# Optimization experiments

Measured on AMD Instinct MI355X. Metric: run time of the kernel, lower is better.

## Reference

```python
import jax, jax.numpy as jnp
import numpy as np

D_IN, D, K, N_CLASSES = 384, 512, 6, 2
SCALE = D ** (-0.5)

def _linear_params(key, fan_in, fan_out):
    kw, kb = jax.random.split(key)
    w = jax.random.normal(kw, (fan_in, fan_out), jnp.float32) * 0.02
    b = jax.random.normal(kb, (fan_out,), jnp.float32) * 0.01
    return w, b

def setup_inputs() -> dict:
    key = jax.random.key(0)
    ks = jax.random.split(key, 10)
    x = jax.random.normal(ks[0], (16384, D_IN), jnp.float32)
    fc1_w, fc1_b = _linear_params(ks[1], D_IN, D)
    wh_w, wh_b = _linear_params(ks[2], D, D)
    wt_w, wt_b = _linear_params(ks[3], D, D)
    lin1_w, lin1_b = _linear_params(ks[4], D, D)
    lin2_w, lin2_b = _linear_params(ks[5], D, D)
    att1_w, att1_b = _linear_params(ks[6], D, D // 2)
    att2_w, att2_b = _linear_params(ks[7], D // 2, 1)
    ln_g = jnp.ones((D,), jnp.float32)
    ln_b = jnp.zeros((D,), jnp.float32)
    fc_w, fc_b = _linear_params(ks[8], D, N_CLASSES)
    return dict(x=x, fc1_w=fc1_w, fc1_b=fc1_b, wh_w=wh_w, wh_b=wh_b,
                wt_w=wt_w, wt_b=wt_b, lin1_w=lin1_w, lin1_b=lin1_b,
                lin2_w=lin2_w, lin2_b=lin2_b, att1_w=att1_w, att1_b=att1_b,
                att2_w=att2_w, att2_b=att2_b, ln_g=ln_g, ln_b=ln_b,
                fc_w=fc_w, fc_b=fc_b)

def _forward(x, fc1_w, fc1_b, wh_w, wh_b, wt_w, wt_b, lin1_w, lin1_b,
             lin2_w, lin2_b, att1_w, att1_b, att2_w, att2_b, ln_g, ln_b,
             fc_w, fc_b):
    lrelu = jax.nn.leaky_relu  # slope 0.01, matches nn.LeakyReLU default
    h = lrelu(x @ fc1_w + fc1_b)                    # [N, D]
    h = (h + h.mean(axis=0, keepdims=True)) * 0.5
    e_h = h @ wh_w + wh_b                           # [N, D]
    e_t = h @ wt_w + wt_b                           # [N, D]
    attn_logit = (e_h * SCALE) @ e_t.T              # [N, N]
    topk_w, topk_i = jax.lax.top_k(attn_logit, K)   # [N, K]
    Nb = e_t[topk_i]                                # gather neighbors [N, K, D]
    p = jax.nn.softmax(topk_w, axis=-1)             # [N, K]
    eh_r = p[..., None] * Nb + (1.0 - p)[..., None] * e_h[:, None, :]
    gate = jnp.tanh(e_h[:, None, :] + eh_r)         # [N, K, D]
    # faithful to torch.einsum('ijkl,ijkm->ijk', Nb, gate): product of sums
    ka_w = Nb.sum(axis=-1) * gate.sum(axis=-1)      # [N, K]
    ka_p = jax.nn.softmax(ka_w, axis=-1)
    e_Nh = jnp.einsum('nk,nkd->nd', ka_p, Nb)       # [N, D]
    sum_emb = lrelu((e_h + e_Nh) @ lin1_w + lin1_b)
    bi_emb = lrelu((e_h * e_Nh) @ lin2_w + lin2_b)
    emb = sum_emb + bi_emb                          # [N, D] (dropout=eval, identity)
    # GlobalAttention readout
    a = lrelu(emb @ att1_w + att1_b) @ att2_w + att2_b  # [N, 1]
    g = jax.nn.softmax(a, axis=0)
    pooled = (g * emb).sum(axis=0, keepdims=True)   # [1, D]
    mu = pooled.mean(axis=-1, keepdims=True)
    var = pooled.var(axis=-1, keepdims=True)
    normed = (pooled - mu) * jax.lax.rsqrt(var + 1e-5) * ln_g + ln_b
    logits = normed @ fc_w + fc_b                   # [1, n_classes]
    return logits

def reference(x, fc1_w, fc1_b, wh_w, wh_b, wt_w, wt_b, lin1_w, lin1_b,
              lin2_w, lin2_b, att1_w, att1_b, att2_w, att2_b, ln_g, ln_b,
              fc_w, fc_b):
    logits = _forward(x, fc1_w, fc1_b, wh_w, wh_b, wt_w, wt_b, lin1_w, lin1_b,
                      lin2_w, lin2_b, att1_w, att1_b, att2_w, att2_b,
                      ln_g, ln_b, fc_w, fc_b)
    y_prob = jax.nn.softmax(logits, axis=-1)
    return logits, y_prob
```

## Files before the change

### kernel.cpp

```cpp
#include <hip/hip_runtime.h>
#include <math.h>

#define NROWS 16384
#define DIN   384
#define DIM   512
#define KSEL  6
#define NSPLIT 4
#define COLS_PER_SPLIT (NROWS / NSPLIT)
#define ATT_SCALE 0.044194173824159216f

typedef unsigned short u16;
typedef __attribute__((ext_vector_type(8))) short bf16x8;
typedef __attribute__((ext_vector_type(16))) float f32x16;

static __device__ __forceinline__ float lrelu_f(float v) {
  return v > 0.f ? v : 0.01f * v;
}

static __device__ __forceinline__ u16 f2bf(float f) {
  unsigned u = __float_as_uint(f);
  unsigned r = (u + 0x7FFFu + ((u >> 16) & 1u)) >> 16;
  return (u16)r;
}

static __device__ __forceinline__ void sbar() {
  asm volatile("" ::: "memory");
  __builtin_amdgcn_s_barrier();
  asm volatile("" ::: "memory");
}

__global__ __launch_bounds__(256)
void convx(const float* __restrict__ X, u16* __restrict__ Xb) {
  int i = blockIdx.x * 256 + threadIdx.x;
  const float4* p = (const float4*)X + (size_t)i * 2;
  float4 a = p[0], b = p[1];
  uint4 o;
  o.x = f2bf(a.x) | ((unsigned)f2bf(a.y) << 16);
  o.y = f2bf(a.z) | ((unsigned)f2bf(a.w) << 16);
  o.z = f2bf(b.x) | ((unsigned)f2bf(b.y) << 16);
  o.w = f2bf(b.z) | ((unsigned)f2bf(b.w) << 16);
  ((uint4*)Xb)[i] = o;
}

__global__ __launch_bounds__(256)
void wconv(const float* __restrict__ W, u16* __restrict__ Wt, int K, int N) {
  int t = blockIdx.x * 256 + threadIdx.x;
  if (t >= K * N) return;
  int k = t / N, n = t - k * N;
  Wt[(size_t)n * K + k] = f2bf(W[t]);
}

__global__ __launch_bounds__(256)
void colsum_partial(const float* __restrict__ H, float* __restrict__ part) {
  int col = blockIdx.x * 64 + (threadIdx.x & 63);
  int sub = threadIdx.x >> 6;
  int rEnd = blockIdx.y * 512 + 512;
  float s = 0.f;
  for (int r = blockIdx.y * 512 + sub; r < rEnd; r += 4)
    s += H[(size_t)r * DIM + col];
  __shared__ float sh[4][64];
  sh[sub][threadIdx.x & 63] = s;
  __syncthreads();
  if (threadIdx.x < 64) {
    float tot = sh[0][threadIdx.x] + sh[1][threadIdx.x] +
                sh[2][threadIdx.x] + sh[3][threadIdx.x];
    part[(size_t)blockIdx.y * DIM + col] = tot;
  }
}

__global__ void finalize_mean(const float* __restrict__ part,
                              float* __restrict__ mean) {
  int c = threadIdx.x;
  float s = 0.f;
  for (int j = 0; j < 32; j++) s += part[j * DIM + c];
  mean[c] = s * (1.0f / NROWS);
}

__global__ __launch_bounds__(256)
void h_fix_bf(const float* __restrict__ H0, const float* __restrict__ mean,
              u16* __restrict__ Hb) {
  int idx = blockIdx.x * 256 + threadIdx.x;
  int c = (idx * 8) & (DIM - 1);
  const float4* p = (const float4*)H0 + (size_t)idx * 2;
  float4 a = p[0], b = p[1];
  float4 m0 = *(const float4*)(mean + c);
  float4 m1 = *(const float4*)(mean + c + 4);
  a.x = (a.x + m0.x) * 0.5f; a.y = (a.y + m0.y) * 0.5f;
  a.z = (a.z + m0.z) * 0.5f; a.w = (a.w + m0.w) * 0.5f;
  b.x = (b.x + m1.x) * 0.5f; b.y = (b.y + m1.y) * 0.5f;
  b.z = (b.z + m1.z) * 0.5f; b.w = (b.w + m1.w) * 0.5f;
  uint4 o;
  o.x = f2bf(a.x) | ((unsigned)f2bf(a.y) << 16);
  o.y = f2bf(a.z) | ((unsigned)f2bf(a.w) << 16);
  o.z = f2bf(b.x) | ((unsigned)f2bf(b.y) << 16);
  o.w = f2bf(b.z) | ((unsigned)f2bf(b.w) << 16);
  ((uint4*)Hb)[idx] = o;
}

template<int ACT, int ACCUM, int STOREBF>
__global__ __launch_bounds__(256, 2)
void gemm_bf16(const u16* __restrict__ A, const u16* __restrict__ Wt,
               const float* __restrict__ bias, float* __restrict__ C,
               u16* __restrict__ Cb, float bscale, int K, int N) {
  __shared__ char lds[65536];
  const int tid = threadIdx.x;
  const int w = tid >> 6, l = tid & 63;
  const int l31 = l & 31, lh = l >> 5, lh16 = lh << 4;
  const int qg = w & 1, ng = w >> 1;
  const int swz = (l31 & 7) << 4;
  const int rowBase = blockIdx.y * 128;
  const int colBase = blockIdx.x * 128;
  const int nsteps = K >> 6;

  f32x16 z;
  #pragma unroll
  for (int i = 0; i < 16; i++) z[i] = 0.f;
  f32x16 acc00 = z, acc01 = z, acc10 = z, acc11 = z;

#define GSTAGE(buf_, kc_) do { \
    const int r_ = tid >> 3, j_ = tid & 7; \
    const int js_ = ((j_ ^ (r_ & 7)) << 3); \
    const u16* as_ = A + (size_t)rowBase * K + (kc_); \
    const u16* ws_ = Wt + (size_t)colBase * K + (kc_); \
    char* ab_ = lds + (buf_) * 16384; \
    char* wb_ = lds + 32768 + (buf_) * 16384; \
    _Pragma("unroll") \
    for (int p_ = 0; p_ < 4; ++p_) { \
      __builtin_amdgcn_global_load_lds( \
        (const __attribute__((address_space(1))) void*)(as_ + (size_t)(r_ + 32 * p_) * K + js_), \
        (__attribute__((address_space(3))) void*)(ab_ + w * 1024 + p_ * 4096), 16, 0, 0); \
      __builtin_amdgcn_global_load_lds( \
        (const __attribute__((address_space(1))) void*)(ws_ + (size_t)(r_ + 32 * p_) * K + js_), \
        (__attribute__((address_space(3))) void*)(wb_ + w * 1024 + p_ * 4096), 16, 0, 0); \
    } \
  } while (0)

  GSTAGE(0, 0);
  asm volatile("s_waitcnt vmcnt(0)" ::: "memory");
  sbar();
  #pragma unroll 1
  for (int s = 0; s < nsteps; ++s) {
    const int cur = s & 1;
    if (s + 1 < nsteps) GSTAGE(cur ^ 1, (s + 1) * 64);
    __builtin_amdgcn_sched_barrier(0);
    const char* ab = lds + cur * 16384;
    const char* wb = lds + 32768 + cur * 16384;
    __builtin_amdgcn_s_setprio(1);
    #pragma unroll
    for (int s4 = 0; s4 < 4; ++s4) {
      const int off = (s4 * 32 + lh16) ^ swz;
      bf16x8 am0 = *(const bf16x8*)(ab + (qg * 64 + l31) * 128 + off);
      bf16x8 am1 = *(const bf16x8*)(ab + (qg * 64 + 32 + l31) * 128 + off);
      bf16x8 wn0 = *(const bf16x8*)(wb + (ng * 64 + l31) * 128 + off);
      bf16x8 wn1 = *(const bf16x8*)(wb + (ng * 64 + 32 + l31) * 128 + off);
      acc00 = __builtin_amdgcn_mfma_f32_32x32x16_bf16(wn0, am0, acc00, 0, 0, 0);
      acc01 = __builtin_amdgcn_mfma_f32_32x32x16_bf16(wn1, am0, acc01, 0, 0, 0);
      acc10 = __builtin_amdgcn_mfma_f32_32x32x16_bf16(wn0, am1, acc10, 0, 0, 0);
      acc11 = __builtin_amdgcn_mfma_f32_32x32x16_bf16(wn1, am1, acc11, 0, 0, 0);
    }
    __builtin_amdgcn_s_setprio(0);
    asm volatile("s_waitcnt vmcnt(0)" ::: "memory");
    sbar();
  }
#undef GSTAGE

  float* Ls = (float*)lds;
  {
    const int m0 = qg * 64 + l31;
    const int k0 = (m0 & 7) << 2;
    #pragma unroll
    for (int r = 0; r < 16; ++r) {
      const int nd = ng * 64 + (r & 3) + 8 * (r >> 2) + 4 * lh;
      Ls[m0 * 128 + (nd ^ k0)] = acc00[r];
      Ls[m0 * 128 + ((nd + 32) ^ k0)] = acc01[r];
      Ls[(m0 + 32) * 128 + (nd ^ k0)] = acc10[r];
      Ls[(m0 + 32) * 128 + ((nd + 32) ^ k0)] = acc11[r];
    }
  }
  sbar();
  #pragma unroll
  for (int p = 0; p < 16; ++p) {
    int idx = tid + 256 * p;
    int m = idx >> 5, c4 = (idx & 31) << 2;
    float4 v = *(const float4*)&Ls[m * 128 + (c4 ^ ((m & 7) << 2))];
    int col = colBase + c4;
    float4 bv = *(const float4*)&bias[col];
    v.x += bv.x; v.y += bv.y; v.z += bv.z; v.w += bv.w;
    if (ACT) {
      v.x = lrelu_f(v.x); v.y = lrelu_f(v.y);
      v.z = lrelu_f(v.z); v.w = lrelu_f(v.w);
    }
    size_t o = (size_t)(rowBase + m) * N + col;
    if (ACCUM) {
      float4 c0 = *(const float4*)&C[o];
      v.x += c0.x; v.y += c0.y; v.z += c0.z; v.w += c0.w;
    }
    *(float4*)&C[o] = v;
    if (STOREBF) {
      ushort4 q;
      q.x = f2bf(v.x * bscale); q.y = f2bf(v.y * bscale);
      q.z = f2bf(v.z * bscale); q.w = f2bf(v.w * bscale);
      *(ushort4*)&Cb[o] = q;
    }
  }
}

#define T6(tv, tix, vv, cc) do { float v_ = (vv); \
  if (v_ > tv[5]) { tv[5] = v_; tix[5] = (cc); \
    if (tv[5] > tv[4]) { float t=tv[4];tv[4]=tv[5];tv[5]=t; int q=tix[4];tix[4]=tix[5];tix[5]=q; } \
    if (tv[4] > tv[3]) { float t=tv[3];tv[3]=tv[4];tv[4]=t; int q=tix[3];tix[3]=tix[4];tix[4]=q; } \
    if (tv[3] > tv[2]) { float t=tv[2];tv[2]=tv[3];tv[3]=t; int q=tix[2];tix[2]=tix[3];tix[3]=q; } \
    if (tv[2] > tv[1]) { float t=tv[1];tv[1]=tv[2];tv[2]=t; int q=tix[1];tix[1]=tix[2];tix[2]=q; } \
    if (tv[1] > tv[0]) { float t=tv[0];tv[0]=tv[1];tv[1]=t; int q=tix[0];tix[0]=tix[1];tix[1]=q; } \
  } } while (0)

__global__ __launch_bounds__(256, 2)
void attn_topk_mfma(const u16* __restrict__ EHb, const u16* __restrict__ ETb,
                    float* __restrict__ TWp, int* __restrict__ TIp) {
  __shared__ char lds[65536];
  const int tid = threadIdx.x;
  const int w = tid >> 6, l = tid & 63;
  const int l31 = l & 31, lh = l >> 5;

  const int bid = blockIdx.x;
  const int xcd = bid & 7;
  const int split = xcd & 3;
  const int rowBase = ((xcd >> 2) * 64 + (bid >> 3)) * 128;
  const int qrow = rowBase + w * 32 + l31;

  bf16x8 areg[32];
  {
    const u16* ap = EHb + (size_t)qrow * DIM + lh * 8;
    #pragma unroll
    for (int ks = 0; ks < 32; ++ks)
      areg[ks] = *(const bf16x8*)(ap + ks * 16);
  }

  char* ldsw = lds + w * 16384;

  f32x16 z;
  #pragma unroll
  for (int i = 0; i < 16; i++) z[i] = 0.f;
  f32x16 acc0 = z, acc1 = z;

  float tv[KSEL]; int tix[KSEL];
  #pragma unroll
  for (int k = 0; k < KSEL; k++) { tv[k] = -INFINITY; tix[k] = 0x7fffffff; }

#define STAGE(buf_, ct_, kc_) do { \
    char* db_ = ldsw + (buf_) * 8192; \
    const u16* bs_ = ETb + (size_t)(split * COLS_PER_SPLIT + (ct_) * 64) * DIM + (kc_) * 64; \
    _Pragma("unroll") \
    for (int p_ = 0; p_ < 8; ++p_) { \
      const int rn_ = p_ * 8 + (l >> 3); \
      const int js_ = ((l & 7) ^ (rn_ & 7)) * 8; \
      __builtin_amdgcn_global_load_lds( \
        (const __attribute__((address_space(1))) void*)(bs_ + (size_t)rn_ * DIM + js_), \
        (__attribute__((address_space(3))) void*)(db_ + p_ * 1024), 16, 0, 0); \
    } \
  } while (0)

  STAGE(0, 0, 0);
  STAGE(1, 0, 1);
  asm volatile("s_waitcnt vmcnt(8)" ::: "memory");

  #pragma unroll 1
  for (int ct = 0; ct < 64; ++ct) {
    #pragma unroll
    for (int kc = 0; kc < 8; ++kc) {
      const char* db = ldsw + (kc & 1) * 8192;
      __builtin_amdgcn_s_setprio(1);
      #pragma unroll
      for (int s4 = 0; s4 < 4; ++s4) {
        const int c0 = ((s4 * 2 + lh) ^ (l31 & 7)) * 16;
        bf16x8 bn0 = *(const bf16x8*)(db + l31 * 128 + c0);
        const int r1 = 32 + l31;
        const int c1 = ((s4 * 2 + lh) ^ (r1 & 7)) * 16;
        bf16x8 bn1 = *(const bf16x8*)(db + r1 * 128 + c1);
        acc0 = __builtin_amdgcn_mfma_f32_32x32x16_bf16(bn0, areg[kc * 4 + s4], acc0, 0, 0, 0);
        acc1 = __builtin_amdgcn_mfma_f32_32x32x16_bf16(bn1, areg[kc * 4 + s4], acc1, 0, 0, 0);
      }
      __builtin_amdgcn_s_setprio(0);
      __builtin_amdgcn_sched_barrier(0);
      if (!(ct == 63 && kc >= 6)) {
        const int nct = (kc < 6) ? ct : ct + 1;
        const int nkc = (kc + 2) & 7;
        STAGE(kc & 1, nct, nkc);
      }
      if (ct == 63 && kc >= 5) { asm volatile("s_waitcnt vmcnt(0)" ::: "memory"); }
      else                     { asm volatile("s_waitcnt vmcnt(8)" ::: "memory"); }
    }
    {
      const int cb = split * COLS_PER_SPLIT + ct * 64 + 4 * lh;
      #pragma unroll
      for (int r = 0; r < 16; ++r) {
        const int nd = cb + (r & 3) + 8 * (r >> 2);
        T6(tv, tix, acc0[r], nd);
        T6(tv, tix, acc1[r], nd + 32);
      }
      acc0 = z; acc1 = z;
    }
  }
#undef STAGE

  {
    float pv[KSEL]; int pi[KSEL];
    #pragma unroll
    for (int k = 0; k < KSEL; k++) {
      pv[k] = __shfl_xor(tv[k], 32);
      pi[k] = __shfl_xor(tix[k], 32);
    }
    #pragma unroll
    for (int k = 0; k < KSEL; k++) {
      float cv = pv[k]; int ci = pi[k];
      if ((cv > tv[5]) || (cv == tv[5] && ci < tix[5])) {
        tv[5] = cv; tix[5] = ci;
        if ((tv[5] > tv[4]) || (tv[5] == tv[4] && tix[5] < tix[4])) {
          float t = tv[4]; tv[4] = tv[5]; tv[5] = t;
          int q = tix[4]; tix[4] = tix[5]; tix[5] = q; }
        if ((tv[4] > tv[3]) || (tv[4] == tv[3] && tix[4] < tix[3])) {
          float t = tv[3]; tv[3] = tv[4]; tv[4] = t;
          int q = tix[3]; tix[3] = tix[4]; tix[4] = q; }
        if ((tv[3] > tv[2]) || (tv[3] == tv[2] && tix[3] < tix[2])) {
          float t = tv[2]; tv[2] = tv[3]; tv[3] = t;
          int q = tix[2]; tix[2] = tix[3]; tix[3] = q; }
        if ((tv[2] > tv[1]) || (tv[2] == tv[1] && tix[2] < tix[1])) {
          float t = tv[1]; tv[1] = tv[2]; tv[2] = t;
          int q = tix[1]; tix[1] = tix[2]; tix[2] = q; }
        if ((tv[1] > tv[0]) || (tv[1] == tv[0] && tix[1] < tix[0])) {
          float t = tv[0]; tv[0] = tv[1]; tv[1] = t;
          int q = tix[0]; tix[0] = tix[1]; tix[1] = q; }
      }
    }
  }
  if (lh == 0) {
    size_t o = ((size_t)split * NROWS + qrow) * KSEL;
    #pragma unroll
    for (int k = 0; k < KSEL; k++) { TWp[o + k] = tv[k]; TIp[o + k] = tix[k]; }
  }
}

__global__ __launch_bounds__(256)
void topk_merge(const float* __restrict__ TWp, const int* __restrict__ TIp,
                float* __restrict__ TW, int* __restrict__ TI) {
  int row = blockIdx.x * 256 + threadIdx.x;
  float tv[KSEL]; int tix[KSEL];
  #pragma unroll
  for (int k = 0; k < KSEL; k++) { tv[k] = -INFINITY; tix[k] = 0x7fffffff; }
  #pragma unroll
  for (int s = 0; s < NSPLIT; s++) {
    size_t o = ((size_t)s * NROWS + row) * KSEL;
    #pragma unroll
    for (int k = 0; k < KSEL; k++) {
      float cv = TWp[o + k]; int ci = TIp[o + k];
      bool better5 = (cv > tv[5]) || (cv == tv[5] && ci < tix[5]);
      if (better5) {
        tv[5] = cv; tix[5] = ci;
        if ((tv[5] > tv[4]) || (tv[5] == tv[4] && tix[5] < tix[4])) {
          float t = tv[4]; tv[4] = tv[5]; tv[5] = t;
          int ti = tix[4]; tix[4] = tix[5]; tix[5] = ti; }
        if ((tv[4] > tv[3]) || (tv[4] == tv[3] && tix[4] < tix[3])) {
          float t = tv[3]; tv[3] = tv[4]; tv[4] = t;
          int ti = tix[3]; tix[3] = tix[4]; tix[4] = ti; }
        if ((tv[3] > tv[2]) || (tv[3] == tv[2] && tix[3] < tix[2])) {
          float t = tv[2]; tv[2] = tv[3]; tv[3] = t;
          int ti = tix[2]; tix[2] = tix[3]; tix[3] = ti; }
        if ((tv[2] > tv[1]) || (tv[2] == tv[1] && tix[2] < tix[1])) {
          float t = tv[1]; tv[1] = tv[2]; tv[2] = t;
          int ti = tix[1]; tix[1] = tix[2]; tix[2] = ti; }
        if ((tv[1] > tv[0]) || (tv[1] == tv[0] && tix[1] < tix[0])) {
          float t = tv[0]; tv[0] = tv[1]; tv[1] = t;
          int ti = tix[0]; tix[0] = tix[1]; tix[1] = ti; }
      }
    }
  }
  size_t o = (size_t)row * KSEL;
  #pragma unroll
  for (int k = 0; k < KSEL; k++) { TW[o + k] = tv[k]; TI[o + k] = tix[k]; }
}

__global__ __launch_bounds__(256)
void neighbor_kernel(const float* __restrict__ EH, const float* __restrict__ ET,
                     const float* __restrict__ TW, const int* __restrict__ TI,
                     u16* __restrict__ SINb, u16* __restrict__ BINb) {
  const int lane = threadIdx.x & 63;
  const int row = blockIdx.x * 4 + (threadIdx.x >> 6);
  const float* eh = EH + (size_t)row * DIM;
  float ehv[8];
  #pragma unroll
  for (int u = 0; u < 8; u++) ehv[u] = eh[u * 64 + lane];
  float tw[KSEL]; int ti[KSEL];
  #pragma unroll
  for (int k = 0; k < KSEL; k++) {
    tw[k] = TW[(size_t)row * KSEL + k];
    ti[k] = TI[(size_t)row * KSEL + k];
  }
  float m = tw[0];
  #pragma unroll
  for (int k = 1; k < KSEL; k++) m = fmaxf(m, tw[k]);
  float p[KSEL], ps = 0.f;
  #pragma unroll
  for (int k = 0; k < KSEL; k++) { p[k] = expf(tw[k] - m); ps += p[k]; }
  float inv = 1.f / ps;
  #pragma unroll
  for (int k = 0; k < KSEL; k++) p[k] *= inv;

  float nb[KSEL][8];
  float kaw[KSEL];
  #pragma unroll
  for (int k = 0; k < KSEL; k++) {
    const float* et = ET + (size_t)ti[k] * DIM;
    float snb = 0.f, sg = 0.f;
    #pragma unroll
    for (int u = 0; u < 8; u++) {
      float nbv = et[u * 64 + lane];
      nb[k][u] = nbv;
      float ehr = p[k] * nbv + (1.f - p[k]) * ehv[u];
      float g = tanhf(ehv[u] + ehr);
      snb += nbv; sg += g;
    }
    #pragma unroll
    for (int off = 32; off > 0; off >>= 1) {
      snb += __shfl_xor(snb, off);
      sg  += __shfl_xor(sg, off);
    }
    kaw[k] = snb * sg;
  }
  float km = kaw[0];
  #pragma unroll
  for (int k = 1; k < KSEL; k++) km = fmaxf(km, kaw[k]);
  float kp[KSEL], ks = 0.f;
  #pragma unroll
  for (int k = 0; k < KSEL; k++) { kp[k] = expf(kaw[k] - km); ks += kp[k]; }
  float kinv = 1.f / ks;
  #pragma unroll
  for (int k = 0; k < KSEL; k++) kp[k] *= kinv;

  #pragma unroll
  for (int u = 0; u < 8; u++) {
    float enh = 0.f;
    #pragma unroll
    for (int k = 0; k < KSEL; k++) enh += kp[k] * nb[k][u];
    size_t o = (size_t)row * DIM + u * 64 + lane;
    SINb[o] = f2bf(ehv[u] + enh);
    BINb[o] = f2bf(ehv[u] * enh);
  }
}

__global__ __launch_bounds__(256)
void att2_kernel(const float* __restrict__ HID, const float* __restrict__ w2,
                 const float* __restrict__ b2, float* __restrict__ ASC) {
  const int lane = threadIdx.x & 63;
  const int row = blockIdx.x * 4 + (threadIdx.x >> 6);
  float4 hv = ((const float4*)(HID + (size_t)row * 256))[lane];
  float4 wv = ((const float4*)w2)[lane];
  float s = hv.x * wv.x + hv.y * wv.y + hv.z * wv.z + hv.w * wv.w;
  #pragma unroll
  for (int off = 32; off > 0; off >>= 1) s += __shfl_xor(s, off);
  if (lane == 0) ASC[row] = s + b2[0];
}

__global__ __launch_bounds__(1024)
void areduce(const float* __restrict__ ASC, float* __restrict__ stats) {
  __shared__ float sm[1024];
  int t = threadIdx.x;
  float m = -INFINITY;
  for (int i = t; i < NROWS; i += 1024) m = fmaxf(m, ASC[i]);
  sm[t] = m; __syncthreads();
  for (int s = 512; s > 0; s >>= 1) {
    if (t < s) sm[t] = fmaxf(sm[t], sm[t + s]);
    __syncthreads();
  }
  float mx = sm[0]; __syncthreads();
  float sum = 0.f;
  for (int i = t; i < NROWS; i += 1024) sum += expf(ASC[i] - mx);
  sm[t] = sum; __syncthreads();
  for (int s = 512; s > 0; s >>= 1) {
    if (t < s) sm[t] += sm[t + s];
    __syncthreads();
  }
  if (t == 0) { stats[0] = mx; stats[1] = sm[0]; }
}

__global__ __launch_bounds__(256)
void pooled_partial(const float* __restrict__ EMB, const float* __restrict__ ASC,
                    const float* __restrict__ stats, float* __restrict__ part) {
  int col = blockIdx.x * 64 + (threadIdx.x & 63);
  int sub = threadIdx.x >> 6;
  float mx = stats[0];
  int rEnd = blockIdx.y * 512 + 512;
  float s = 0.f;
  for (int r = blockIdx.y * 512 + sub; r < rEnd; r += 4)
    s += expf(ASC[r] - mx) * EMB[(size_t)r * DIM + col];
  __shared__ float sh[4][64];
  sh[sub][threadIdx.x & 63] = s;
  __syncthreads();
  if (threadIdx.x < 64) {
    float tot = sh[0][threadIdx.x] + sh[1][threadIdx.x] +
                sh[2][threadIdx.x] + sh[3][threadIdx.x];
    part[(size_t)blockIdx.y * DIM + col] = tot;
  }
}

__global__ __launch_bounds__(512)
void final_kernel(const float* __restrict__ part, const float* __restrict__ stats,
                  const float* __restrict__ ln_g, const float* __restrict__ ln_b,
                  const float* __restrict__ fc_w, const float* __restrict__ fc_b,
                  float* __restrict__ out) {
  __shared__ float sh[512];
  int t = threadIdx.x;
  float s = 0.f;
  for (int j = 0; j < 32; j++) s += part[j * DIM + t];
  float pooled = s / stats[1];
  sh[t] = pooled; __syncthreads();
  for (int off = 256; off > 0; off >>= 1) {
    if (t < off) sh[t] += sh[t + off];
    __syncthreads();
  }
  float mu = sh[0] * (1.f / DIM); __syncthreads();
  float dv = pooled - mu;
  sh[t] = dv * dv; __syncthreads();
  for (int off = 256; off > 0; off >>= 1) {
    if (t < off) sh[t] += sh[t + off];
    __syncthreads();
  }
  float var = sh[0] * (1.f / DIM); __syncthreads();
  float normed = dv * rsqrtf(var + 1e-5f) * ln_g[t] + ln_b[t];
  sh[t] = normed * fc_w[t * 2 + 0]; __syncthreads();
  for (int off = 256; off > 0; off >>= 1) {
    if (t < off) sh[t] += sh[t + off];
    __syncthreads();
  }
  float l0 = sh[0] + fc_b[0]; __syncthreads();
  sh[t] = normed * fc_w[t * 2 + 1]; __syncthreads();
  for (int off = 256; off > 0; off >>= 1) {
    if (t < off) sh[t] += sh[t + off];
    __syncthreads();
  }
  float l1 = sh[0] + fc_b[1];
  if (t == 0) {
    float mm = fmaxf(l0, l1);
    float e0 = expf(l0 - mm), e1 = expf(l1 - mm);
    float si = 1.f / (e0 + e1);
    out[0] = l0; out[1] = l1; out[2] = e0 * si; out[3] = e1 * si;
  }
}

extern "C" void kernel_launch(void* const* d_in, const int* in_sizes, int n_in,
                              void* d_out, int out_size, void* d_ws, size_t ws_size,
                              hipStream_t stream) {
  (void)in_sizes; (void)n_in; (void)out_size; (void)ws_size;
  const float* x      = (const float*)d_in[0];
  const float* fc1_w  = (const float*)d_in[1];
  const float* fc1_b  = (const float*)d_in[2];
  const float* wh_w   = (const float*)d_in[3];
  const float* wh_b   = (const float*)d_in[4];
  const float* wt_w   = (const float*)d_in[5];
  const float* wt_b   = (const float*)d_in[6];
  const float* lin1_w = (const float*)d_in[7];
  const float* lin1_b = (const float*)d_in[8];
  const float* lin2_w = (const float*)d_in[9];
  const float* lin2_b = (const float*)d_in[10];
  const float* att1_w = (const float*)d_in[11];
  const float* att1_b = (const float*)d_in[12];
  const float* att2_w = (const float*)d_in[13];
  const float* att2_b = (const float*)d_in[14];
  const float* ln_g   = (const float*)d_in[15];
  const float* ln_b   = (const float*)d_in[16];
  const float* fc_w   = (const float*)d_in[17];
  const float* fc_b   = (const float*)d_in[18];
  float* out = (float*)d_out;

  char* ws = (char*)d_ws;
  float* B0   = (float*)(ws);
  float* B1   = (float*)(ws + 33554432);
  float* B2   = (float*)(ws + 67108864);
  float* TWp  = (float*)(ws + 100663296);
  int*   TIp  = (int*)  (ws + 100663296 + 1572864);
  float* TW   = (float*)(ws + 100663296 + 3145728);
  int*   TI   = (int*)  (ws + 100663296 + 3145728 + 393216);
  float* part = (float*)(ws + 100663296 + 3145728 + 786432);
  float* mean = (float*)(ws + 100663296 + 3145728 + 786432 + 65536);
  float* ascr = (float*)(ws + 100663296 + 3145728 + 786432 + 65536 + 2048);
  float* stats= (float*)(ws + 100663296 + 3145728 + 786432 + 65536 + 2048 + 65536);
  u16*   hb   = (u16*)(ws + 104732672);
  u16*   EHb  = (u16*)(ws + 104732672 + 16777216);
  u16*   ETb  = (u16*)(ws + 104732672 + 33554432);
  u16*   WT   = (u16*)(ws + 104732672 + 50331648);
  u16* fc1t = WT;
  u16* wht  = fc1t + 196608;
  u16* wtt  = wht + 262144;
  u16* lin1t= wtt + 262144;
  u16* lin2t= lin1t + 262144;
  u16* att1t= lin2t + 262144;
  u16* xb   = (u16*)B1;
  u16* sinb = EHb;
  u16* binb = ETb;
  u16* embb = hb;

  convx<<<3072, 256, 0, stream>>>(x, xb);
  wconv<<<768, 256, 0, stream>>>(fc1_w, fc1t, 384, 512);
  wconv<<<1024, 256, 0, stream>>>(wh_w, wht, 512, 512);
  wconv<<<1024, 256, 0, stream>>>(wt_w, wtt, 512, 512);
  wconv<<<1024, 256, 0, stream>>>(lin1_w, lin1t, 512, 512);
  wconv<<<1024, 256, 0, stream>>>(lin2_w, lin2t, 512, 512);
  wconv<<<512, 256, 0, stream>>>(att1_w, att1t, 512, 256);
  gemm_bf16<1,0,0><<<dim3(4,128), 256, 0, stream>>>(xb, fc1t, fc1_b, B0, nullptr, 1.f, 384, 512);
  colsum_partial<<<dim3(8,32), 256, 0, stream>>>(B0, part);
  finalize_mean<<<1, 512, 0, stream>>>(part, mean);
  h_fix_bf<<<4096, 256, 0, stream>>>(B0, mean, hb);
  gemm_bf16<0,0,1><<<dim3(4,128), 256, 0, stream>>>(hb, wht, wh_b, B1, EHb, ATT_SCALE, 512, 512);
  gemm_bf16<0,0,1><<<dim3(4,128), 256, 0, stream>>>(hb, wtt, wt_b, B2, ETb, 1.f, 512, 512);
  attn_topk_mfma<<<512, 256, 0, stream>>>(EHb, ETb, TWp, TIp);
  topk_merge<<<64, 256, 0, stream>>>(TWp, TIp, TW, TI);
  neighbor_kernel<<<4096, 256, 0, stream>>>(B1, B2, TW, TI, sinb, binb);
  gemm_bf16<1,0,0><<<dim3(4,128), 256, 0, stream>>>(sinb, lin1t, lin1_b, B2, nullptr, 1.f, 512, 512);
  gemm_bf16<1,1,1><<<dim3(4,128), 256, 0, stream>>>(binb, lin2t, lin2_b, B2, embb, 1.f, 512, 512);
  gemm_bf16<1,0,0><<<dim3(2,128), 256, 0, stream>>>(embb, att1t, att1_b, B0, nullptr, 1.f, 512, 256);
  att2_kernel<<<4096, 256, 0, stream>>>(B0, att2_w, att2_b, ascr);
  areduce<<<1, 1024, 0, stream>>>(ascr, stats);
  pooled_partial<<<dim3(8,32), 256, 0, stream>>>(B2, ascr, stats, part);
  final_kernel<<<1, 512, 0, stream>>>(part, stats, ln_g, ln_b, fc_w, fc_b, out);
}
```

Baseline: 667.1 us.

## Share ET tiles across warps via block-wide triple-buffered LDS staging

Previously each of the four warps staged its own private copy of the same ET tile into LDS, using 64KB per block. The tiles are now loaded cooperatively by all 256 threads into a shared 3-slot ring buffer of 24KB, with a block barrier each step. The top-k update is also moved inside the kc==7 step, ahead of the prefetch. This cuts redundant global-to-LDS traffic by about four times and frees LDS for occupancy, in exchange for a block-wide barrier on every k-chunk.

```diff
diff --git a/kernel.cpp b/kernel.cpp
--- a/kernel.cpp
+++ b/kernel.cpp
@@ -217,7 +217,7 @@
 __global__ __launch_bounds__(256, 2)
 void attn_topk_mfma(const u16* __restrict__ EHb, const u16* __restrict__ ETb,
                     float* __restrict__ TWp, int* __restrict__ TIp) {
-  __shared__ char lds[65536];
+  __shared__ char lds[24576];
   const int tid = threadIdx.x;
   const int w = tid >> 6, l = tid & 63;
   const int l31 = l & 31, lh = l >> 5;
@@ -236,8 +236,6 @@
       areg[ks] = *(const bf16x8*)(ap + ks * 16);
   }
 
-  char* ldsw = lds + w * 16384;
-
   f32x16 z;
   #pragma unroll
   for (int i = 0; i < 16; i++) z[i] = 0.f;
@@ -247,28 +245,32 @@
   #pragma unroll
   for (int k = 0; k < KSEL; k++) { tv[k] = -INFINITY; tix[k] = 0x7fffffff; }
 
-#define STAGE(buf_, ct_, kc_) do { \
-    char* db_ = ldsw + (buf_) * 8192; \
-    const u16* bs_ = ETb + (size_t)(split * COLS_PER_SPLIT + (ct_) * 64) * DIM + (kc_) * 64; \
+#define STAGE(bufi_, ph_) do { \
+    const int ct_ = (ph_) >> 3, kc_ = (ph_) & 7; \
+    char* db_ = lds + (bufi_) * 8192; \
+    const u16* bs_ = ETb + (size_t)(split * COLS_PER_SPLIT + ct_ * 64) * DIM + kc_ * 64; \
     _Pragma("unroll") \
-    for (int p_ = 0; p_ < 8; ++p_) { \
-      const int rn_ = p_ * 8 + (l >> 3); \
-      const int js_ = ((l & 7) ^ (rn_ & 7)) * 8; \
+    for (int p_ = 0; p_ < 2; ++p_) { \
+      const int c_ = tid + 256 * p_; \
+      const int rn_ = c_ >> 3; \
+      const int js_ = (((c_ & 7) ^ (rn_ & 7)) << 3); \
       __builtin_amdgcn_global_load_lds( \
         (const __attribute__((address_space(1))) void*)(bs_ + (size_t)rn_ * DIM + js_), \
-        (__attribute__((address_space(3))) void*)(db_ + p_ * 1024), 16, 0, 0); \
+        (__attribute__((address_space(3))) void*)(db_ + w * 1024 + p_ * 4096), 16, 0, 0); \
     } \
   } while (0)
 
-  STAGE(0, 0, 0);
-  STAGE(1, 0, 1);
-  asm volatile("s_waitcnt vmcnt(8)" ::: "memory");
+  int bufr = 0;
+  STAGE(0, 0);
+  STAGE(1, 1);
+  asm volatile("s_waitcnt vmcnt(2)" ::: "memory");
 
   #pragma unroll 1
   for (int ct = 0; ct < 64; ++ct) {
     #pragma unroll
     for (int kc = 0; kc < 8; ++kc) {
-      const char* db = ldsw + (kc & 1) * 8192;
+      sbar();
+      const char* db = lds + bufr * 8192;
       __builtin_amdgcn_s_setprio(1);
       #pragma unroll
       for (int s4 = 0; s4 < 4; ++s4) {
@@ -281,24 +283,27 @@
         acc1 = __builtin_amdgcn_mfma_f32_32x32x16_bf16(bn1, areg[kc * 4 + s4], acc1, 0, 0, 0);
       }
       __builtin_amdgcn_s_setprio(0);
+      if (kc == 7) {
+        const int cb = split * COLS_PER_SPLIT + ct * 64 + 4 * lh;
+        #pragma unroll
+        for (int r = 0; r < 16; ++r) {
+          const int nd = cb + (r & 3) + 8 * (r >> 2);
+          T6(tv, tix, acc0[r], nd);
+          T6(tv, tix, acc1[r], nd + 32);
+        }
+        acc0 = z; acc1 = z;
+      }
       __builtin_amdgcn_sched_barrier(0);
-      if (!(ct == 63 && kc >= 6)) {
-        const int nct = (kc < 6) ? ct : ct + 1;
-        const int nkc = (kc + 2) & 7;
-        STAGE(kc & 1, nct, nkc);
+      {
+        const int p = ct * 8 + kc;
+        if (p + 2 < 512) {
+          const int bs = (bufr >= 1) ? bufr - 1 : bufr + 2;
+          STAGE(bs, p + 2);
+        }
+        if (p < 510) { asm volatile("s_waitcnt vmcnt(2)" ::: "memory"); }
+        else         { asm volatile("s_waitcnt vmcnt(0)" ::: "memory"); }
       }
-      if (ct == 63 && kc >= 5) { asm volatile("s_waitcnt vmcnt(0)" ::: "memory"); }
-      else                     { asm volatile("s_waitcnt vmcnt(8)" ::: "memory"); }
-    }
-    {
-      const int cb = split * COLS_PER_SPLIT + ct * 64 + 4 * lh;
-      #pragma unroll
-      for (int r = 0; r < 16; ++r) {
-        const int nd = cb + (r & 3) + 8 * (r >> 2);
-        T6(tv, tix, acc0[r], nd);
-        T6(tv, tix, acc1[r], nd + 32);
-      }
-      acc0 = z; acc1 = z;
+      bufr = (bufr == 2) ? 0 : bufr + 1;
     }
   }
 #undef STAGE
```

Result: faster. 598.9 us (-10.2%).
